# Performance work log

Hardware: AMD Instinct MI355X
Metric: run time of the kernel (lower is better)

The kernel has to match this reference:

```python
import jax, jax.numpy as jnp
import numpy as np

B, T, C = 2, 2048, 1024
NH = 16
HD = C // NH

def setup_inputs() -> dict:
    key = jax.random.key(0)
    ks = jax.random.split(key, 4)
    x = jax.random.normal(ks[0], (B, T, C), dtype=jnp.float32)
    w_attn = jax.random.normal(ks[1], (C, 3 * C), dtype=jnp.float32) * (1.0 / np.sqrt(C))
    b_attn = jnp.zeros((3 * C,), dtype=jnp.float32)
    w_proj = jax.random.normal(ks[2], (C, C), dtype=jnp.float32) * (1.0 / np.sqrt(C))
    b_proj = jnp.zeros((C,), dtype=jnp.float32)
    return {"x": x, "w_attn": w_attn, "b_attn": b_attn, "w_proj": w_proj, "b_proj": b_proj}

def reference(x, w_attn, b_attn, w_proj, b_proj):
    Bq, Tq, Cq = x.shape
    qkv = x @ w_attn + b_attn                      # [B,T,3C]
    q, k, v = jnp.split(qkv, 3, axis=2)
    # [B,T,C] -> [B,NH,T,HD]
    def heads(t):
        return t.reshape(Bq, Tq, NH, HD).transpose(0, 2, 1, 3)
    q, k, v = heads(q), heads(k), heads(v)
    att = jnp.einsum('bhqd,bhkd->bhqk', q, k) * (1.0 / np.sqrt(HD))
    causal = jnp.tril(jnp.ones((Tq, Tq), dtype=bool))
    att = jnp.where(causal[None, None], att, -jnp.inf)
    att = jax.nn.softmax(att, axis=-1)
    y = jnp.einsum('bhqk,bhkd->bhqd', att, v)      # [B,NH,T,HD]
    y = y.transpose(0, 2, 1, 3).reshape(Bq, Tq, Cq)
    return y @ w_proj + b_proj
```

## Files before the change

### kernel.cpp

```cpp
#include <hip/hip_runtime.h>

typedef unsigned short u16;
typedef short bf16x8 __attribute__((ext_vector_type(8)));
typedef float f32x4 __attribute__((ext_vector_type(4)));

#define BATCH 2
#define SEQ   2048
#define CH    1024
#define NHEAD 16
#define HDIM  64
#define ROWS  (BATCH*SEQ)

#define SWZ(r_, c_) (((r_)*64) + ((c_) ^ (((r_)&7)*8)))

__device__ __forceinline__ u16 f2b(float f) {
  unsigned u = __builtin_bit_cast(unsigned, f);
  u += 0x7FFFu + ((u >> 16) & 1u);
  return (u16)(u >> 16);
}
__device__ __forceinline__ float b2f(u16 h) {
  unsigned u = ((unsigned)h) << 16;
  return __builtin_bit_cast(float, u);
}
__device__ __forceinline__ float exp2_fast(float x) {
  float r; asm("v_exp_f32 %0, %1" : "=v"(r) : "v"(x)); return r;
}
__device__ __forceinline__ unsigned cvt_pk_bf16(float a, float b) {
  unsigned r; asm("v_cvt_pk_bf16_f32 %0, %1, %2" : "=v"(r) : "v"(a), "v"(b)); return r;
}

__device__ __forceinline__ void gload_lds16(const void* g, void* l) {
  __builtin_amdgcn_global_load_lds(
      (const __attribute__((address_space(1))) unsigned int*)g,
      (__attribute__((address_space(3))) unsigned int*)l, 16, 0, 0);
}

__global__ void csa_convert_x(const float* __restrict__ in, u16* __restrict__ out,
                              int n8) {
  int i = blockIdx.x * 256 + threadIdx.x;
  if (i >= n8) return;
  const float4* f4 = (const float4*)in;
  float4 v0 = f4[2*i], v1 = f4[2*i+1];
  ushort4 o0, o1;
  o0.x = f2b(v0.x); o0.y = f2b(v0.y); o0.z = f2b(v0.z); o0.w = f2b(v0.w);
  o1.x = f2b(v1.x); o1.y = f2b(v1.y); o1.z = f2b(v1.z); o1.w = f2b(v1.w);
  ((ushort4*)out)[2*i]   = o0;
  ((ushort4*)out)[2*i+1] = o1;
}

__global__ void csa_transpose2(const float* __restrict__ wa, const float* __restrict__ wp,
                               u16* __restrict__ wat, u16* __restrict__ wpt) {
  __shared__ float tile[32][33];
  int bx = blockIdx.x;
  const float* in; u16* out; int C;
  if (bx < 96) { in = wa; out = wat; C = 3*CH; }
  else         { in = wp; out = wpt; C = CH; bx -= 96; }
  const int R = CH;
  const int bxc = bx * 32, by = blockIdx.y * 32;
  const int tx = threadIdx.x, ty = threadIdx.y;
  #pragma unroll
  for (int j = 0; j < 4; ++j) {
    int r = by + ty + j*8, c = bxc + tx;
    tile[ty + j*8][tx] = in[(size_t)r*C + c];
  }
  __syncthreads();
  #pragma unroll
  for (int j = 0; j < 4; ++j) {
    int oc = bxc + ty + j*8;
    int orr = by + tx;
    out[(size_t)oc*R + orr] = f2b(tile[tx][ty + j*8]);
  }
}

__global__ __launch_bounds__(512) void csa_gemm_qkv(
    const u16* __restrict__ A, const u16* __restrict__ Bt,
    const float* __restrict__ bias,
    u16* __restrict__ qbo, u16* __restrict__ kb, u16* __restrict__ vtb)
{
  __shared__ __align__(16) u16 As[2][256*64];
  __shared__ __align__(16) u16 Bs[2][192*64];
  const int t = threadIdx.x, lane = t & 63, w = t >> 6;
  const int wm = w >> 2, wn = w & 3, g = lane >> 4, qi = lane & 15;

  const int wgid = blockIdx.y * 16 + blockIdx.x;
  const int c8 = wgid & 7, inner = wgid >> 3;
  const int bm = (c8 >> 1) * 4 + (inner >> 3);
  const int bn = (c8 & 1) * 8 + (inner & 7);

  f32x4 acc[8][3] = {};

  const u16* Ab = A  + (size_t)(bm*256)*CH;
  const u16* Bb = Bt + (size_t)(bn*192)*CH;
  const int srow = t >> 3;
  const int scol = (t & 7) * 8;

  #pragma unroll
  for (int p = 0; p < 4; ++p)
    gload_lds16(Ab + (size_t)(p*64 + srow)*CH + scol, &As[0][p*4096 + w*512]);
  #pragma unroll
  for (int p = 0; p < 3; ++p)
    gload_lds16(Bb + (size_t)(p*64 + srow)*CH + scol, &Bs[0][p*4096 + w*512]);
  __syncthreads();

  int cur = 0;
  for (int k0 = 0; k0 < CH; k0 += 64) {
    if (k0 + 64 < CH) {
      #pragma unroll
      for (int p = 0; p < 4; ++p)
        gload_lds16(Ab + (size_t)(p*64 + srow)*CH + (k0+64) + scol, &As[cur^1][p*4096 + w*512]);
      #pragma unroll
      for (int p = 0; p < 3; ++p)
        gload_lds16(Bb + (size_t)(p*64 + srow)*CH + (k0+64) + scol, &Bs[cur^1][p*4096 + w*512]);
    }
    #pragma unroll
    for (int kk = 0; kk < 2; ++kk) {
      bf16x8 af[8], bfr[3];
      #pragma unroll
      for (int m = 0; m < 8; ++m)
        af[m] = *(const bf16x8*)&As[cur][(wm*128 + m*16 + qi)*64 + kk*32 + g*8];
      #pragma unroll
      for (int n = 0; n < 3; ++n)
        bfr[n] = *(const bf16x8*)&Bs[cur][(wn*48 + n*16 + qi)*64 + kk*32 + g*8];
      #pragma unroll
      for (int m = 0; m < 8; ++m)
        #pragma unroll
        for (int n = 0; n < 3; ++n)
          acc[m][n] = __builtin_amdgcn_mfma_f32_16x16x32_bf16(af[m], bfr[n], acc[m][n], 0, 0, 0);
    }
    __syncthreads();
    cur ^= 1;
  }

  #pragma unroll
  for (int m = 0; m < 8; ++m) {
    const int row0 = bm*256 + wm*128 + m*16 + g*4;
    const int bb = row0 >> 11;
    const int t0 = row0 & 2047;
    #pragma unroll
    for (int n = 0; n < 3; ++n) {
      const int col = bn*192 + wn*48 + n*16 + qi;
      const float bv = bias[col];
      const int which = col >> 10;
      const int cc = col & 1023;
      const int h = cc >> 6, d = cc & 63;
      const int bh = bb*16 + h;
      if (which == 2) {
        ushort4 pw;
        pw.x = f2b(acc[m][n][0] + bv);
        pw.y = f2b(acc[m][n][1] + bv);
        pw.z = f2b(acc[m][n][2] + bv);
        pw.w = f2b(acc[m][n][3] + bv);
        *(ushort4*)&vtb[((size_t)bh*HDIM + d)*SEQ + t0] = pw;
      } else {
        u16* dst = (which == 0) ? qbo : kb;
        #pragma unroll
        for (int r = 0; r < 4; ++r)
          dst[((size_t)bh*SEQ + t0 + r)*HDIM + d] = f2b(acc[m][n][r] + bv);
      }
    }
  }
}

__global__ __launch_bounds__(256) void csa_gemm_proj(
    const u16* __restrict__ A, const u16* __restrict__ Bt,
    const float* __restrict__ bias, float* __restrict__ out)
{
  __shared__ __align__(16) u16 As[2][128*64];
  __shared__ __align__(16) u16 Bs[2][128*64];
  const int t = threadIdx.x, lane = t & 63, w = t >> 6;
  const int wm = w >> 1, wn = w & 1, g = lane >> 4, qi = lane & 15;
  const int bm = blockIdx.y, bn = blockIdx.x;

  f32x4 acc[4][4] = {};

  const u16* Ab = A  + (size_t)(bm*128)*CH;
  const u16* Bb = Bt + (size_t)(bn*128)*CH;
  const int srow = t >> 3;
  const int scol = (t & 7) * 8;

  #pragma unroll
  for (int p = 0; p < 4; ++p) {
    gload_lds16(Ab + (size_t)(p*32 + srow)*CH + scol, &As[0][p*2048 + w*512]);
    gload_lds16(Bb + (size_t)(p*32 + srow)*CH + scol, &Bs[0][p*2048 + w*512]);
  }
  __syncthreads();

  int cur = 0;
  for (int k0 = 0; k0 < CH; k0 += 64) {
    if (k0 + 64 < CH) {
      #pragma unroll
      for (int p = 0; p < 4; ++p) {
        gload_lds16(Ab + (size_t)(p*32 + srow)*CH + (k0+64) + scol, &As[cur^1][p*2048 + w*512]);
        gload_lds16(Bb + (size_t)(p*32 + srow)*CH + (k0+64) + scol, &Bs[cur^1][p*2048 + w*512]);
      }
    }
    #pragma unroll
    for (int kk = 0; kk < 2; ++kk) {
      bf16x8 af[4], bfr[4];
      #pragma unroll
      for (int m = 0; m < 4; ++m)
        af[m] = *(const bf16x8*)&As[cur][(wm*64 + m*16 + qi)*64 + kk*32 + g*8];
      #pragma unroll
      for (int n = 0; n < 4; ++n)
        bfr[n] = *(const bf16x8*)&Bs[cur][(wn*64 + n*16 + qi)*64 + kk*32 + g*8];
      #pragma unroll
      for (int m = 0; m < 4; ++m)
        #pragma unroll
        for (int n = 0; n < 4; ++n)
          acc[m][n] = __builtin_amdgcn_mfma_f32_16x16x32_bf16(af[m], bfr[n], acc[m][n], 0, 0, 0);
    }
    __syncthreads();
    cur ^= 1;
  }

  #pragma unroll
  for (int m = 0; m < 4; ++m) {
    const int row0 = bm*128 + wm*64 + m*16 + g*4;
    #pragma unroll
    for (int n = 0; n < 4; ++n) {
      const int col = bn*128 + wn*64 + n*16 + qi;
      const float bv = bias[col];
      #pragma unroll
      for (int r = 0; r < 4; ++r)
        out[(size_t)(row0 + r)*CH + col] = acc[m][n][r] + bv;
    }
  }
}

__global__ __launch_bounds__(512) void csa_attn(
    const u16* __restrict__ qb, const u16* __restrict__ kb,
    const u16* __restrict__ vtb, u16* __restrict__ yout)
{
  const int bh = blockIdx.x, pair = blockIdx.y;
  const int bidx = bh >> 4, h = bh & 15;
  const int t = threadIdx.x, lane = t & 63, w = t >> 6;
  const int g = lane >> 4, qi = lane & 15;
  __shared__ __align__(16) u16 Ks[2][128*64];
  __shared__ __align__(16) u16 Vs[2][64*128];
  __shared__ __align__(16) u16 Ps[8][2][16*64];

  const size_t kvbase = (size_t)bh * SEQ * HDIM;
  const u16* kb_bh  = kb  + kvbase;
  const u16* vtb_bh = vtb + kvbase;

  const int krow_  = t >> 3;
  const int kcolsw = ((t & 7) * 8) ^ ((krow_ & 7) * 8);
  const int vd_    = t >> 4;
  const int vcolsw = ((t & 15) * 8) ^ ((vd_ & 15) * 8);

  int offKb[2][4], offVb[2][4], offPw[4], offPr[2];
  #pragma unroll
  for (int c = 0; c < 2; ++c) {
    offPr[c] = qi*64 + ((c*32 + g*8) ^ ((qi & 7) * 8));
    #pragma unroll
    for (int s4 = 0; s4 < 4; ++s4)
      offKb[c][s4] = (s4*16 + qi)*64 + ((c*32 + g*8) ^ ((qi & 7) * 8));
    #pragma unroll
    for (int nf = 0; nf < 4; ++nf)
      offVb[c][nf] = (nf*16 + qi)*128 + ((c*32 + g*8) ^ (qi * 8));
  }
  #pragma unroll
  for (int s4 = 0; s4 < 4; ++s4)
    offPw[s4] = qi*64 + ((s4*16 + g*4) ^ ((qi & 7) * 8));

  const float QSCALE = 0.18033688011112042f;
  const int lqa = w*16 + qi;

  for (int half = 0; half < 2; ++half) {
    const int qt = half ? (15 - pair) : pair;
    const int qrow = qt*128 + w*16;
    const int ntile = qt + 1;

    bf16x8 qf[2];
    #pragma unroll
    for (int c = 0; c < 2; ++c) {
      qf[c] = *(const bf16x8*)&qb[(kvbase + (size_t)(qrow + qi)*HDIM) + c*32 + g*8];
      #pragma unroll
      for (int e = 0; e < 8; ++e)
        qf[c][e] = (short)f2b(b2f((u16)qf[c][e]) * QSCALE);
    }

    f32x4 yacc[4] = {};
    float mrun = -1e30f, srun = 0.f;

    __syncthreads();
    {
      const u16* kp = kb_bh;
      gload_lds16(kp + (size_t)krow_*64 + kcolsw,        &Ks[0][       w*512]);
      gload_lds16(kp + (size_t)(64 + krow_)*64 + kcolsw, &Ks[0][4096 + w*512]);
      const u16* vp = vtb_bh;
      gload_lds16(vp + (size_t)vd_*SEQ + vcolsw,         &Vs[0][       w*512]);
      gload_lds16(vp + (size_t)(32 + vd_)*SEQ + vcolsw,  &Vs[0][4096 + w*512]);
    }
    __syncthreads();

    int buf = 0;
    for (int kt = 0; kt < ntile; ++kt) {
      if (kt + 1 < ntile) {
        const u16* kp = kb_bh + (size_t)((kt + 1) * 128) * 64;
        gload_lds16(kp + (size_t)krow_*64 + kcolsw,        &Ks[buf^1][       w*512]);
        gload_lds16(kp + (size_t)(64 + krow_)*64 + kcolsw, &Ks[buf^1][4096 + w*512]);
        const u16* vp = vtb_bh + (kt + 1) * 128;
        gload_lds16(vp + (size_t)vd_*SEQ + vcolsw,         &Vs[buf^1][       w*512]);
        gload_lds16(vp + (size_t)(32 + vd_)*SEQ + vcolsw,  &Vs[buf^1][4096 + w*512]);
      }

      f32x4 sa[4] = {}, sb[4] = {};
      #pragma unroll
      for (int c = 0; c < 2; ++c)
        #pragma unroll
        for (int s4 = 0; s4 < 4; ++s4) {
          bf16x8 ka = *(const bf16x8*)&Ks[buf][offKb[c][s4]];
          sa[s4] = __builtin_amdgcn_mfma_f32_16x16x32_bf16(ka, qf[c], sa[s4], 0, 0, 0);
        }
      #pragma unroll
      for (int c = 0; c < 2; ++c)
        #pragma unroll
        for (int s4 = 0; s4 < 4; ++s4) {
          bf16x8 kbv = *(const bf16x8*)&Ks[buf][4096 + offKb[c][s4]];
          sb[s4] = __builtin_amdgcn_mfma_f32_16x16x32_bf16(kbv, qf[c], sb[s4], 0, 0, 0);
        }

      if (kt == ntile - 1) {
        #pragma unroll
        for (int s4 = 0; s4 < 4; ++s4)
          #pragma unroll
          for (int r = 0; r < 4; ++r) {
            const int lk = s4*16 + g*4 + r;
            if (lk > lqa)      sa[s4][r] = -3.0e38f;
            if (lk > lqa - 64) sb[s4][r] = -3.0e38f;
          }
      }

      float tmax = sa[0][0];
      #pragma unroll
      for (int s4 = 0; s4 < 4; ++s4)
        #pragma unroll
        for (int r = 0; r < 4; ++r) {
          tmax = fmaxf(tmax, sa[s4][r]);
          tmax = fmaxf(tmax, sb[s4][r]);
        }
      if (!__all(tmax - mrun <= 11.5f)) {
        float tmf = fmaxf(tmax, __shfl_xor(tmax, 16));
        tmf = fmaxf(tmf, __shfl_xor(tmf, 32));
        float mnew = fmaxf(mrun, tmf);
        float fac = exp2_fast(mrun - mnew);
        #pragma unroll
        for (int r = 0; r < 4; ++r) {
          float fr = __shfl(fac, g*4 + r);
          #pragma unroll
          for (int nf = 0; nf < 4; ++nf) yacc[nf][r] *= fr;
        }
        srun *= fac;
        mrun = mnew;
      }
      float tsum = 0.f;
      #pragma unroll
      for (int s4 = 0; s4 < 4; ++s4)
        #pragma unroll
        for (int r = 0; r < 4; ++r) {
          float pa = exp2_fast(sa[s4][r] - mrun);
          float pb = exp2_fast(sb[s4][r] - mrun);
          sa[s4][r] = pa; sb[s4][r] = pb;
          tsum += pa + pb;
        }
      srun += tsum;

      #pragma unroll
      for (int s4 = 0; s4 < 4; ++s4) {
        uint2 pwa, pwb;
        pwa.x = cvt_pk_bf16(sa[s4][0], sa[s4][1]);
        pwa.y = cvt_pk_bf16(sa[s4][2], sa[s4][3]);
        pwb.x = cvt_pk_bf16(sb[s4][0], sb[s4][1]);
        pwb.y = cvt_pk_bf16(sb[s4][2], sb[s4][3]);
        *(uint2*)&Ps[w][0][offPw[s4]] = pwa;
        *(uint2*)&Ps[w][1][offPw[s4]] = pwb;
      }

      #pragma unroll
      for (int c = 0; c < 2; ++c) {
        bf16x8 pa0 = *(const bf16x8*)&Ps[w][0][offPr[c]];
        bf16x8 pb0 = *(const bf16x8*)&Ps[w][1][offPr[c]];
        #pragma unroll
        for (int nf = 0; nf < 4; ++nf) {
          bf16x8 va = *(const bf16x8*)&Vs[buf][offVb[c][nf]];
          yacc[nf] = __builtin_amdgcn_mfma_f32_16x16x32_bf16(pa0, va, yacc[nf], 0, 0, 0);
          bf16x8 vb = *(const bf16x8*)&Vs[buf][offVb[c][nf] ^ 64];
          yacc[nf] = __builtin_amdgcn_mfma_f32_16x16x32_bf16(pb0, vb, yacc[nf], 0, 0, 0);
        }
      }

      __syncthreads();
      buf ^= 1;
    }

    float srf = srun + __shfl_xor(srun, 16);
    srf += __shfl_xor(srf, 32);
    #pragma unroll
    for (int r = 0; r < 4; ++r) {
      float sv = __shfl(srf, g*4 + r);
      float inv = 1.f / sv;
      int qg = qrow + g*4 + r;
      #pragma unroll
      for (int nf = 0; nf < 4; ++nf) {
        int d = nf*16 + qi;
        yout[((size_t)bidx*SEQ + qg)*CH + h*HDIM + d] = f2b(yacc[nf][r] * inv);
      }
    }
  }
}

extern "C" void kernel_launch(void* const* d_in, const int* in_sizes, int n_in,
                              void* d_out, int out_size, void* d_ws, size_t ws_size,
                              hipStream_t stream) {
  (void)in_sizes; (void)n_in; (void)out_size; (void)ws_size;
  const float* x      = (const float*)d_in[0];
  const float* w_attn = (const float*)d_in[1];
  const float* b_attn = (const float*)d_in[2];
  const float* w_proj = (const float*)d_in[3];
  const float* b_proj = (const float*)d_in[4];

  char* ws = (char*)d_ws;
  const size_t MB = 1024*1024;
  u16* xb  = (u16*)(ws);
  u16* wat = (u16*)(ws +  8*MB);
  u16* wpt = (u16*)(ws + 14*MB);
  u16* qb  = (u16*)(ws + 16*MB);
  u16* kb  = (u16*)(ws + 24*MB);
  u16* vtb = (u16*)(ws + 32*MB);

  csa_convert_x<<<2048, 256, 0, stream>>>(x, xb, ROWS*CH/8);
  csa_transpose2<<<dim3(128, 32), dim3(32, 8), 0, stream>>>(w_attn, w_proj, wat, wpt);
  csa_gemm_qkv<<<dim3(16, 16), 512, 0, stream>>>(xb, wat, b_attn, qb, kb, vtb);
  csa_attn<<<dim3(32, 8), 512, 0, stream>>>(qb, kb, vtb, xb);
  csa_gemm_proj<<<dim3(8, 32), 256, 0, stream>>>(xb, wpt, b_proj, (float*)d_out);
}
```

Baseline: 110.9 us.

## Triple-buffer A tiles with XOR-swizzled LDS and merge prep kernels

Both GEMMs now keep A tiles three stages deep and B tiles double-buffered, using explicit vmcnt waits and raw barriers instead of __syncthreads, so global-to-LDS loads run further ahead of the MFMA work. LDS columns are XOR-swizzled by row on both the store and the read side to cut bank conflicts on fragment loads. The x conversion and weight transpose kernels are fused into one launch to save a kernel launch. The hand-counted vmcnt values and the larger LDS footprint are fragile and may lower occupancy.

```diff
diff --git a/kernel.cpp b/kernel.cpp
--- a/kernel.cpp
+++ b/kernel.cpp
@@ -11,7 +11,7 @@
 #define HDIM  64
 #define ROWS  (BATCH*SEQ)
 
-#define SWZ(r_, c_) (((r_)*64) + ((c_) ^ (((r_)&7)*8)))
+#define WAITV(N) asm volatile("s_waitcnt vmcnt(" #N ")" ::: "memory")
 
 __device__ __forceinline__ u16 f2b(float f) {
   unsigned u = __builtin_bit_cast(unsigned, f);
@@ -35,39 +35,41 @@
       (__attribute__((address_space(3))) unsigned int*)l, 16, 0, 0);
 }
 
-__global__ void csa_convert_x(const float* __restrict__ in, u16* __restrict__ out,
-                              int n8) {
-  int i = blockIdx.x * 256 + threadIdx.x;
-  if (i >= n8) return;
-  const float4* f4 = (const float4*)in;
-  float4 v0 = f4[2*i], v1 = f4[2*i+1];
-  ushort4 o0, o1;
-  o0.x = f2b(v0.x); o0.y = f2b(v0.y); o0.z = f2b(v0.z); o0.w = f2b(v0.w);
-  o1.x = f2b(v1.x); o1.y = f2b(v1.y); o1.z = f2b(v1.z); o1.w = f2b(v1.w);
-  ((ushort4*)out)[2*i]   = o0;
-  ((ushort4*)out)[2*i+1] = o1;
-}
-
-__global__ void csa_transpose2(const float* __restrict__ wa, const float* __restrict__ wp,
-                               u16* __restrict__ wat, u16* __restrict__ wpt) {
+__global__ void csa_prep(const float* __restrict__ x,
+                         const float* __restrict__ wa, const float* __restrict__ wp,
+                         u16* __restrict__ xb, u16* __restrict__ wat,
+                         u16* __restrict__ wpt) {
   __shared__ float tile[32][33];
-  int bx = blockIdx.x;
+  const int b = blockIdx.x, t = threadIdx.x;
+  if (b < 2048) {
+    int i = b * 256 + t;
+    const float4* f4 = (const float4*)x;
+    float4 v0 = f4[2*i], v1 = f4[2*i+1];
+    ushort4 o0, o1;
+    o0.x = f2b(v0.x); o0.y = f2b(v0.y); o0.z = f2b(v0.z); o0.w = f2b(v0.w);
+    o1.x = f2b(v1.x); o1.y = f2b(v1.y); o1.z = f2b(v1.z); o1.w = f2b(v1.w);
+    ((ushort4*)xb)[2*i]   = o0;
+    ((ushort4*)xb)[2*i+1] = o1;
+    return;
+  }
+  int bb = b - 2048;
+  int bx = bb & 127, by = bb >> 7;
   const float* in; u16* out; int C;
   if (bx < 96) { in = wa; out = wat; C = 3*CH; }
   else         { in = wp; out = wpt; C = CH; bx -= 96; }
   const int R = CH;
-  const int bxc = bx * 32, by = blockIdx.y * 32;
-  const int tx = threadIdx.x, ty = threadIdx.y;
+  const int bxc = bx * 32, byc = by * 32;
+  const int tx = t & 31, ty = t >> 5;
   #pragma unroll
   for (int j = 0; j < 4; ++j) {
-    int r = by + ty + j*8, c = bxc + tx;
+    int r = byc + ty + j*8, c = bxc + tx;
     tile[ty + j*8][tx] = in[(size_t)r*C + c];
   }
   __syncthreads();
   #pragma unroll
   for (int j = 0; j < 4; ++j) {
     int oc = bxc + ty + j*8;
-    int orr = by + tx;
+    int orr = byc + tx;
     out[(size_t)oc*R + orr] = f2b(tile[tx][ty + j*8]);
   }
 }
@@ -77,10 +79,11 @@
     const float* __restrict__ bias,
     u16* __restrict__ qbo, u16* __restrict__ kb, u16* __restrict__ vtb)
 {
-  __shared__ __align__(16) u16 As[2][256*64];
+  __shared__ __align__(16) u16 As[3][256*64];
   __shared__ __align__(16) u16 Bs[2][192*64];
   const int t = threadIdx.x, lane = t & 63, w = t >> 6;
   const int wm = w >> 2, wn = w & 3, g = lane >> 4, qi = lane & 15;
+  const int xq = (qi & 7) * 8;
 
   const int wgid = blockIdx.y * 16 + blockIdx.x;
   const int c8 = wgid & 7, inner = wgid >> 3;
@@ -92,44 +95,53 @@
   const u16* Ab = A  + (size_t)(bm*256)*CH;
   const u16* Bb = Bt + (size_t)(bn*192)*CH;
   const int srow = t >> 3;
-  const int scol = (t & 7) * 8;
-
-  #pragma unroll
-  for (int p = 0; p < 4; ++p)
-    gload_lds16(Ab + (size_t)(p*64 + srow)*CH + scol, &As[0][p*4096 + w*512]);
-  #pragma unroll
-  for (int p = 0; p < 3; ++p)
-    gload_lds16(Bb + (size_t)(p*64 + srow)*CH + scol, &Bs[0][p*4096 + w*512]);
-  __syncthreads();
-
-  int cur = 0;
-  for (int k0 = 0; k0 < CH; k0 += 64) {
-    if (k0 + 64 < CH) {
-      #pragma unroll
-      for (int p = 0; p < 4; ++p)
-        gload_lds16(Ab + (size_t)(p*64 + srow)*CH + (k0+64) + scol, &As[cur^1][p*4096 + w*512]);
-      #pragma unroll
-      for (int p = 0; p < 3; ++p)
-        gload_lds16(Bb + (size_t)(p*64 + srow)*CH + (k0+64) + scol, &Bs[cur^1][p*4096 + w*512]);
-    }
+  const int scolsw = ((t & 7) * 8) ^ ((srow & 7) * 8);
+
+#define QKV_STAGE_A(kt_, buf_) do { const size_t k_ = (size_t)(kt_)*64;            \
+    gload_lds16(Ab + (size_t)(  0 + srow)*CH + k_ + scolsw, &As[buf_][      w*512]); \
+    gload_lds16(Ab + (size_t)( 64 + srow)*CH + k_ + scolsw, &As[buf_][ 4096+w*512]); \
+    gload_lds16(Ab + (size_t)(128 + srow)*CH + k_ + scolsw, &As[buf_][ 8192+w*512]); \
+    gload_lds16(Ab + (size_t)(192 + srow)*CH + k_ + scolsw, &As[buf_][12288+w*512]); \
+  } while (0)
+#define QKV_STAGE_B(kt_, buf_) do { const size_t k_ = (size_t)(kt_)*64;            \
+    gload_lds16(Bb + (size_t)(  0 + srow)*CH + k_ + scolsw, &Bs[buf_][      w*512]); \
+    gload_lds16(Bb + (size_t)( 64 + srow)*CH + k_ + scolsw, &Bs[buf_][ 4096+w*512]); \
+    gload_lds16(Bb + (size_t)(128 + srow)*CH + k_ + scolsw, &Bs[buf_][ 8192+w*512]); \
+  } while (0)
+
+  QKV_STAGE_A(0, 0); QKV_STAGE_B(0, 0); QKV_STAGE_A(1, 1);
+
+  int a3 = 0;
+  for (int kt = 0; kt < 16; ++kt) {
+    if (kt < 15) QKV_STAGE_B(kt + 1, (kt + 1) & 1);
+    if (kt < 14) { int ab = a3 + 2; if (ab >= 3) ab -= 3; QKV_STAGE_A(kt + 2, ab); }
+    if (kt < 14)       WAITV(11);
+    else if (kt == 14) WAITV(7);
+    else               WAITV(0);
+    __builtin_amdgcn_s_barrier();
+    __builtin_amdgcn_sched_barrier(0);
+    const u16* Ac = &As[a3][0];
+    const u16* Bc = &Bs[kt & 1][0];
     #pragma unroll
     for (int kk = 0; kk < 2; ++kk) {
       bf16x8 af[8], bfr[3];
       #pragma unroll
       for (int m = 0; m < 8; ++m)
-        af[m] = *(const bf16x8*)&As[cur][(wm*128 + m*16 + qi)*64 + kk*32 + g*8];
+        af[m] = *(const bf16x8*)&Ac[(wm*128 + m*16 + qi)*64 + ((kk*32 + g*8) ^ xq)];
       #pragma unroll
       for (int n = 0; n < 3; ++n)
-        bfr[n] = *(const bf16x8*)&Bs[cur][(wn*48 + n*16 + qi)*64 + kk*32 + g*8];
+        bfr[n] = *(const bf16x8*)&Bc[(wn*48 + n*16 + qi)*64 + ((kk*32 + g*8) ^ xq)];
       #pragma unroll
       for (int m = 0; m < 8; ++m)
         #pragma unroll
         for (int n = 0; n < 3; ++n)
           acc[m][n] = __builtin_amdgcn_mfma_f32_16x16x32_bf16(af[m], bfr[n], acc[m][n], 0, 0, 0);
     }
-    __syncthreads();
-    cur ^= 1;
-  }
+    __builtin_amdgcn_s_barrier();
+    a3 = (a3 == 2) ? 0 : a3 + 1;
+  }
+#undef QKV_STAGE_A
+#undef QKV_STAGE_B
 
   #pragma unroll
   for (int m = 0; m < 8; ++m) {
@@ -165,10 +177,11 @@
     const u16* __restrict__ A, const u16* __restrict__ Bt,
     const float* __restrict__ bias, float* __restrict__ out)
 {
-  __shared__ __align__(16) u16 As[2][128*64];
+  __shared__ __align__(16) u16 As[3][128*64];
   __shared__ __align__(16) u16 Bs[2][128*64];
   const int t = threadIdx.x, lane = t & 63, w = t >> 6;
   const int wm = w >> 1, wn = w & 1, g = lane >> 4, qi = lane & 15;
+  const int xq = (qi & 7) * 8;
   const int bm = blockIdx.y, bn = blockIdx.x;
 
   f32x4 acc[4][4] = {};
@@ -176,42 +189,47 @@
   const u16* Ab = A  + (size_t)(bm*128)*CH;
   const u16* Bb = Bt + (size_t)(bn*128)*CH;
   const int srow = t >> 3;
-  const int scol = (t & 7) * 8;
-
-  #pragma unroll
-  for (int p = 0; p < 4; ++p) {
-    gload_lds16(Ab + (size_t)(p*32 + srow)*CH + scol, &As[0][p*2048 + w*512]);
-    gload_lds16(Bb + (size_t)(p*32 + srow)*CH + scol, &Bs[0][p*2048 + w*512]);
-  }
-  __syncthreads();
-
-  int cur = 0;
-  for (int k0 = 0; k0 < CH; k0 += 64) {
-    if (k0 + 64 < CH) {
-      #pragma unroll
-      for (int p = 0; p < 4; ++p) {
-        gload_lds16(Ab + (size_t)(p*32 + srow)*CH + (k0+64) + scol, &As[cur^1][p*2048 + w*512]);
-        gload_lds16(Bb + (size_t)(p*32 + srow)*CH + (k0+64) + scol, &Bs[cur^1][p*2048 + w*512]);
-      }
-    }
+  const int scolsw = ((t & 7) * 8) ^ ((srow & 7) * 8);
+
+#define PRJ_STAGE(P_, base_, kt_, buf_) do { const size_t k_ = (size_t)(kt_)*64;      \
+    gload_lds16(P_ + (size_t)( 0 + srow)*CH + k_ + scolsw, &base_[buf_][     w*512]); \
+    gload_lds16(P_ + (size_t)(32 + srow)*CH + k_ + scolsw, &base_[buf_][2048+w*512]); \
+    gload_lds16(P_ + (size_t)(64 + srow)*CH + k_ + scolsw, &base_[buf_][4096+w*512]); \
+    gload_lds16(P_ + (size_t)(96 + srow)*CH + k_ + scolsw, &base_[buf_][6144+w*512]); \
+  } while (0)
+
+  PRJ_STAGE(Ab, As, 0, 0); PRJ_STAGE(Bb, Bs, 0, 0); PRJ_STAGE(Ab, As, 1, 1);
+
+  int a3 = 0;
+  for (int kt = 0; kt < 16; ++kt) {
+    if (kt < 15) PRJ_STAGE(Bb, Bs, kt + 1, (kt + 1) & 1);
+    if (kt < 14) { int ab = a3 + 2; if (ab >= 3) ab -= 3; PRJ_STAGE(Ab, As, kt + 2, ab); }
+    if (kt < 14)       WAITV(12);
+    else if (kt == 14) WAITV(8);
+    else               WAITV(0);
+    __builtin_amdgcn_s_barrier();
+    __builtin_amdgcn_sched_barrier(0);
+    const u16* Ac = &As[a3][0];
+    const u16* Bc = &Bs[kt & 1][0];
     #pragma unroll
     for (int kk = 0; kk < 2; ++kk) {
       bf16x8 af[4], bfr[4];
       #pragma unroll
       for (int m = 0; m < 4; ++m)
-        af[m] = *(const bf16x8*)&As[cur][(wm*64 + m*16 + qi)*64 + kk*32 + g*8];
+        af[m] = *(const bf16x8*)&Ac[(wm*64 + m*16 + qi)*64 + ((kk*32 + g*8) ^ xq)];
       #pragma unroll
       for (int n = 0; n < 4; ++n)
-        bfr[n] = *(const bf16x8*)&Bs[cur][(wn*64 + n*16 + qi)*64 + kk*32 + g*8];
+        bfr[n] = *(const bf16x8*)&Bc[(wn*64 + n*16 + qi)*64 + ((kk*32 + g*8) ^ xq)];
       #pragma unroll
       for (int m = 0; m < 4; ++m)
         #pragma unroll
         for (int n = 0; n < 4; ++n)
           acc[m][n] = __builtin_amdgcn_mfma_f32_16x16x32_bf16(af[m], bfr[n], acc[m][n], 0, 0, 0);
     }
-    __syncthreads();
-    cur ^= 1;
-  }
+    __builtin_amdgcn_s_barrier();
+    a3 = (a3 == 2) ? 0 : a3 + 1;
+  }
+#undef PRJ_STAGE
 
   #pragma unroll
   for (int m = 0; m < 4; ++m) {
@@ -429,8 +447,7 @@
   u16* kb  = (u16*)(ws + 24*MB);
   u16* vtb = (u16*)(ws + 32*MB);
 
-  csa_convert_x<<<2048, 256, 0, stream>>>(x, xb, ROWS*CH/8);
-  csa_transpose2<<<dim3(128, 32), dim3(32, 8), 0, stream>>>(w_attn, w_proj, wat, wpt);
+  csa_prep<<<6144, 256, 0, stream>>>(x, w_attn, w_proj, xb, wat, wpt);
   csa_gemm_qkv<<<dim3(16, 16), 512, 0, stream>>>(xb, wat, b_attn, qb, kb, vtb);
   csa_attn<<<dim3(32, 8), 512, 0, stream>>>(qb, kb, vtb, xb);
   csa_gemm_proj<<<dim3(8, 32), 256, 0, stream>>>(xb, wpt, b_proj, (float*)d_out);
```

Result: faster. 99.24 us, median of 5 (-10.5%).
